# Kernel optimization log

Hardware: AMD Instinct MI355X
Metric: run time of the kernel (lower is better)

The kernel has to match this reference:

```python
import jax, jax.numpy as jnp
import numpy as np

# Elliptical structuring-element sizes (cv2.MORPH_ELLIPSE-like), per init_kwargs.
KERNEL_SIZES = [3, 5, 7]
B, C, H, W = 16, 1, 1024, 1024
_MAX_VAL = 1e4  # kornia's max_val; geodesic border padding uses +-max_val
_EPS = 1e-7     # smp DiceLoss eps


def _ellipse_offsets(k):
    """Offsets (i, j) within a k x k window where the elliptical mask is 1."""
    r = k // 2
    yy, xx = np.mgrid[-r:r + 1, -r:r + 1]
    rr = max(r, 1)
    mask = (xx / rr) ** 2 + (yy / rr) ** 2 <= 1.0 + 1e-9
    return [(i, j) for i in range(k) for j in range(k) if mask[i, j]]


def _morph(x, k, offsets, is_dilation):
    """Flat morphological dilation (max) / erosion (min) over the ellipse support.
    Matches kornia's unfold-based morphology with geodesic border handling,
    but computed as a fused running max/min over static shifted views (no unfold blow-up)."""
    pad = k // 2
    fill = -_MAX_VAL if is_dilation else _MAX_VAL
    xp = jnp.pad(x, ((0, 0), (0, 0), (pad, pad), (pad, pad)), constant_values=fill)
    h, w = x.shape[-2], x.shape[-1]
    op = jnp.maximum if is_dilation else jnp.minimum
    i0, j0 = offsets[0]
    out = xp[..., i0:i0 + h, j0:j0 + w]
    for (i, j) in offsets[1:]:
        out = op(out, xp[..., i:i + h, j:j + w])
    return out


def _dice_loss(pred, target):
    """smp.losses.DiceLoss(mode='binary', from_logits=False): reduce over dims (batch, pixels)."""
    b = pred.shape[0]
    p = pred.reshape(b, 1, -1)
    t = target.reshape(b, 1, -1)
    inter = jnp.sum(p * t, axis=(0, 2))            # [1]
    card = jnp.sum(p + t, axis=(0, 2))             # [1]
    score = 2.0 * inter / jnp.clip(card, _EPS)
    loss = (1.0 - score) * (jnp.sum(t, axis=(0, 2)) > 0)
    return jnp.mean(loss)


def setup_inputs() -> dict:
    key = jax.random.key(0)
    k1, k2 = jax.random.split(key)
    pred = jax.random.uniform(k1, (B, C, H, W), dtype=jnp.float32)
    teacher = jax.random.uniform(k2, (B, C, H, W), dtype=jnp.float32)
    return {"pred_student_prob": pred, "teacher_prob": teacher}


def reference(pred_student_prob, teacher_prob):
    teacher = jax.lax.stop_gradient(teacher_prob)  # .detach()
    total = jnp.float32(0.0)
    for k in KERNEL_SIZES:
        offs = _ellipse_offsets(k)
        obj_dil = _morph(teacher, k, offs, True)
        obj_ero = _morph(teacher, k, offs, False)
        total = total + _dice_loss(pred_student_prob, obj_dil) + _dice_loss(pred_student_prob, obj_ero)
    return total / len(KERNEL_SIZES)
```

## Files before the change

kernel.cpp:

```cpp
#include <hip/hip_runtime.h>

#define H_ 1024
#define W_ 1024
#define B_ 16
#define TH 8
#define STEPS (TH + 6)
#define GX (H_ / TH)
#define NBLK (GX * B_)
#define NACC 13


__global__ __launch_bounds__(256, 2) void k_partials(const float* __restrict__ pred,
                                                     const float* __restrict__ tch,
                                                     float* __restrict__ partials) {
  const int tid = threadIdx.x;
  const int b   = blockIdx.y;
  const int y0  = blockIdx.x * TH;
  const int x0  = tid * 4;
  const float* tb = tch  + (size_t)b * (H_ * W_);
  const float* pb = pred + (size_t)b * (H_ * W_);

  float acc[NACC];
#pragma unroll
  for (int j = 0; j < NACC; j++) acc[j] = 0.f;

  float h0q[7][4];
  float h3M[5][4], h3N[5][4];
  float h5M[6][4], h5N[6][4];
  float h7M[4][4], h7N[4][4];

#pragma unroll
  for (int s = 0; s < STEPS; ++s) {
    const int t    = y0 + s - 3;
    const int trow = t < 0 ? 0 : (t >= H_ ? H_ - 1 : t);
    const float* tr = tb + (size_t)trow * W_;

    float a[12];
    const float4 cv = *reinterpret_cast<const float4*>(tr + x0);
    a[4] = cv.x; a[5] = cv.y; a[6] = cv.z; a[7] = cv.w;
    if (tid > 0) {
      const float4 lv = *reinterpret_cast<const float4*>(tr + x0 - 4);
      a[0] = lv.x; a[1] = lv.y; a[2] = lv.z; a[3] = lv.w;
    } else {
      a[0] = a[1] = a[2] = a[3] = cv.x;
    }
    if (tid < 255) {
      const float4 rv = *reinterpret_cast<const float4*>(tr + x0 + 4);
      a[8] = rv.x; a[9] = rv.y; a[10] = rv.z; a[11] = rv.w;
    } else {
      a[8] = a[9] = a[10] = a[11] = cv.w;
    }

    float QM[8], QN[8];
#pragma unroll
    for (int i = 1; i <= 7; ++i) {
      QM[i] = fmaxf(fmaxf(a[i], a[i + 1]), a[i + 2]);
      QN[i] = fminf(fminf(a[i], a[i + 1]), a[i + 2]);
    }
#pragma unroll
    for (int c = 0; c < 4; ++c) {
      h0q[s % 7][c] = a[c + 4];
      h3M[s % 5][c] = QM[c + 3];
      h3N[s % 5][c] = QN[c + 3];
      h5M[s % 6][c] = fmaxf(QM[c + 2], QM[c + 4]);
      h5N[s % 6][c] = fminf(QN[c + 2], QN[c + 4]);
      h7M[s % 4][c] = fmaxf(fmaxf(QM[c + 1], QM[c + 4]), a[c + 7]);
      h7N[s % 4][c] = fminf(fminf(QN[c + 1], QN[c + 4]), a[c + 7]);
    }

    if (s >= 6) {
      const int j = s - 6;
      const float4 pv = *reinterpret_cast<const float4*>(pb + (size_t)(y0 + j) * W_ + x0);
      const float p[4] = {pv.x, pv.y, pv.z, pv.w};
#pragma unroll
      for (int c = 0; c < 4; ++c) {
        const float d3v = fmaxf(fmaxf(h3M[(s + 2) % 5][c], h0q[(s + 3) % 7][c]), h0q[(s + 5) % 7][c]);
        const float e3v = fminf(fminf(h3N[(s + 2) % 5][c], h0q[(s + 3) % 7][c]), h0q[(s + 5) % 7][c]);

        float d5v = fmaxf(fmaxf(h5M[(s + 3) % 6][c], h3M[(s + 1) % 5][c]), h3M[(s + 3) % 5][c]);
        d5v = fmaxf(fmaxf(d5v, h0q[(s + 2) % 7][c]), h0q[(s + 6) % 7][c]);
        float e5v = fminf(fminf(h5N[(s + 3) % 6][c], h3N[(s + 1) % 5][c]), h3N[(s + 3) % 5][c]);
        e5v = fminf(fminf(e5v, h0q[(s + 2) % 7][c]), h0q[(s + 6) % 7][c]);

        float d7v = fmaxf(fmaxf(h7M[(s + 1) % 4][c], h5M[(s + 2) % 6][c]), h5M[(s + 4) % 6][c]);
        d7v = fmaxf(fmaxf(d7v, h5M[(s + 1) % 6][c]), h5M[(s + 5) % 6][c]);
        d7v = fmaxf(fmaxf(d7v, h0q[(s + 1) % 7][c]), h0q[s % 7][c]);
        float e7v = fminf(fminf(h7N[(s + 1) % 4][c], h5N[(s + 2) % 6][c]), h5N[(s + 4) % 6][c]);
        e7v = fminf(fminf(e7v, h5N[(s + 1) % 6][c]), h5N[(s + 5) % 6][c]);
        e7v = fminf(fminf(e7v, h0q[(s + 1) % 7][c]), h0q[s % 7][c]);

        acc[0]  += p[c];
        acc[1]  += d3v;  acc[2]  = fmaf(p[c], d3v, acc[2]);
        acc[3]  += e3v;  acc[4]  = fmaf(p[c], e3v, acc[4]);
        acc[5]  += d5v;  acc[6]  = fmaf(p[c], d5v, acc[6]);
        acc[7]  += e5v;  acc[8]  = fmaf(p[c], e5v, acc[8]);
        acc[9]  += d7v;  acc[10] = fmaf(p[c], d7v, acc[10]);
        acc[11] += e7v;  acc[12] = fmaf(p[c], e7v, acc[12]);
      }
    }
  }

#pragma unroll
  for (int j = 0; j < NACC; j++) {
    float v = acc[j];
#pragma unroll
    for (int off = 32; off > 0; off >>= 1) v += __shfl_down(v, off, 64);
    acc[j] = v;
  }
  __shared__ float red[4][NACC];
  const int lane = tid & 63, wv = tid >> 6;
  if (lane == 0) {
#pragma unroll
    for (int j = 0; j < NACC; j++) red[wv][j] = acc[j];
  }
  __syncthreads();
  if (tid == 0) {
    const int bid = blockIdx.y * gridDim.x + blockIdx.x;
#pragma unroll
    for (int j = 0; j < NACC; j++)
      partials[bid * NACC + j] = red[0][j] + red[1][j] + red[2][j] + red[3][j];
  }
}

__global__ __launch_bounds__(256) void k_final(const float* __restrict__ partials,
                                               float* __restrict__ out) {
  double acc[NACC];
#pragma unroll
  for (int j = 0; j < NACC; j++) acc[j] = 0.0;
  for (int i = threadIdx.x; i < NBLK; i += 256) {
#pragma unroll
    for (int j = 0; j < NACC; j++) acc[j] += (double)partials[i * NACC + j];
  }
  __shared__ double red[NACC][256];
#pragma unroll
  for (int j = 0; j < NACC; j++) red[j][threadIdx.x] = acc[j];
  __syncthreads();
  for (int s = 128; s > 0; s >>= 1) {
    if (threadIdx.x < (unsigned)s) {
#pragma unroll
      for (int j = 0; j < NACC; j++) red[j][threadIdx.x] += red[j][threadIdx.x + s];
    }
    __syncthreads();
  }
  if (threadIdx.x == 0) {
    const double Sp = red[0][0];
    double total = 0.0;
#pragma unroll
    for (int k = 0; k < 3; k++) {
      const double Sd = red[1 + 4 * k][0], Id = red[2 + 4 * k][0];
      const double Se = red[3 + 4 * k][0], Ie = red[4 + 4 * k][0];
      double cd = Sp + Sd; if (cd < 1e-7) cd = 1e-7;
      double ce = Sp + Se; if (ce < 1e-7) ce = 1e-7;
      total += (1.0 - 2.0 * Id / cd) * (Sd > 0.0 ? 1.0 : 0.0);
      total += (1.0 - 2.0 * Ie / ce) * (Se > 0.0 ? 1.0 : 0.0);
    }
    out[0] = (float)(total / 3.0);
  }
}

extern "C" void kernel_launch(void* const* d_in, const int* in_sizes, int n_in,
                              void* d_out, int out_size, void* d_ws, size_t ws_size,
                              hipStream_t stream) {
  const float* pred = (const float*)d_in[0];
  const float* tch  = (const float*)d_in[1];
  float* partials = (float*)d_ws;

  k_partials<<<dim3(GX, B_), 256, 0, stream>>>(pred, tch, partials);
  k_final<<<1, 256, 0, stream>>>(partials, (float*)d_out);
}
```

Measured before the change: 164.7 us.

## Split dilation and erosion into separate block halves with taller tiles

Dilation and erosion now run in separate blocks, selected by blockIdx.z through a templated body. This halves the live ring-buffer state per thread so launch bounds can allow 4 blocks per SM instead of 2. The tile height doubles to 16 rows, which cuts the halo re-read overhead. In exchange, teacher and pred are each read twice, once per z-slice, which adds memory traffic. Partials are stored column-major, and the final kernel reduces them with direct loads and wave shuffles instead of a shared-memory tree.

```diff
diff --git a/kernel.cpp b/kernel.cpp
--- a/kernel.cpp
+++ b/kernel.cpp
@@ -3,31 +3,30 @@
 #define H_ 1024
 #define W_ 1024
 #define B_ 16
-#define TH 8
+#define TH 16
 #define STEPS (TH + 6)
 #define GX (H_ / TH)
-#define NBLK (GX * B_)
+#define NB2 (GX * B_)
 #define NACC 13
 
+template<bool M>
+__device__ __forceinline__ float O2(float a, float b) { return M ? fmaxf(a, b) : fminf(a, b); }
+template<bool M>
+__device__ __forceinline__ float O3(float a, float b, float c) {
+  return M ? fmaxf(fmaxf(a, b), c) : fminf(fminf(a, b), c);
+}
 
-__global__ __launch_bounds__(256, 2) void k_partials(const float* __restrict__ pred,
-                                                     const float* __restrict__ tch,
-                                                     float* __restrict__ partials) {
-  const int tid = threadIdx.x;
-  const int b   = blockIdx.y;
-  const int y0  = blockIdx.x * TH;
-  const int x0  = tid * 4;
-  const float* tb = tch  + (size_t)b * (H_ * W_);
-  const float* pb = pred + (size_t)b * (H_ * W_);
+template<bool M>
+__device__ __forceinline__ void morph_body(const float* __restrict__ pb,
+                                           const float* __restrict__ tb,
+                                           float* __restrict__ partials,
+                                           int tid, int y0, int bid) {
+  const int x0 = tid * 4;
+  float acc[7];
+#pragma unroll
+  for (int j = 0; j < 7; j++) acc[j] = 0.f;
 
-  float acc[NACC];
-#pragma unroll
-  for (int j = 0; j < NACC; j++) acc[j] = 0.f;
-
-  float h0q[7][4];
-  float h3M[5][4], h3N[5][4];
-  float h5M[6][4], h5N[6][4];
-  float h7M[4][4], h7N[4][4];
+  float h0q[7][4], h3q[5][4], h5q[6][4], h7q[4][4];
 
 #pragma unroll
   for (int s = 0; s < STEPS; ++s) {
@@ -51,63 +50,101 @@
       a[8] = a[9] = a[10] = a[11] = cv.w;
     }
 
-    float QM[8], QN[8];
+    float Q[8];
 #pragma unroll
-    for (int i = 1; i <= 7; ++i) {
-      QM[i] = fmaxf(fmaxf(a[i], a[i + 1]), a[i + 2]);
-      QN[i] = fminf(fminf(a[i], a[i + 1]), a[i + 2]);
-    }
+    for (int i = 1; i <= 7; ++i) Q[i] = O3<M>(a[i], a[i + 1], a[i + 2]);
 #pragma unroll
     for (int c = 0; c < 4; ++c) {
       h0q[s % 7][c] = a[c + 4];
-      h3M[s % 5][c] = QM[c + 3];
-      h3N[s % 5][c] = QN[c + 3];
-      h5M[s % 6][c] = fmaxf(QM[c + 2], QM[c + 4]);
-      h5N[s % 6][c] = fminf(QN[c + 2], QN[c + 4]);
-      h7M[s % 4][c] = fmaxf(fmaxf(QM[c + 1], QM[c + 4]), a[c + 7]);
-      h7N[s % 4][c] = fminf(fminf(QN[c + 1], QN[c + 4]), a[c + 7]);
+      h3q[s % 5][c] = Q[c + 3];
+      h5q[s % 6][c] = O2<M>(Q[c + 2], Q[c + 4]);
+      h7q[s % 4][c] = O3<M>(Q[c + 1], Q[c + 4], a[c + 7]);
     }
 
     if (s >= 6) {
-      const int j = s - 6;
-      const float4 pv = *reinterpret_cast<const float4*>(pb + (size_t)(y0 + j) * W_ + x0);
+      const float4 pv = *reinterpret_cast<const float4*>(pb + (size_t)(y0 + s - 6) * W_ + x0);
       const float p[4] = {pv.x, pv.y, pv.z, pv.w};
 #pragma unroll
       for (int c = 0; c < 4; ++c) {
-        const float d3v = fmaxf(fmaxf(h3M[(s + 2) % 5][c], h0q[(s + 3) % 7][c]), h0q[(s + 5) % 7][c]);
-        const float e3v = fminf(fminf(h3N[(s + 2) % 5][c], h0q[(s + 3) % 7][c]), h0q[(s + 5) % 7][c]);
+        const float k3 = O3<M>(h3q[(s + 2) % 5][c], h0q[(s + 3) % 7][c], h0q[(s + 5) % 7][c]);
+        float k5 = O3<M>(h5q[(s + 3) % 6][c], h3q[(s + 1) % 5][c], h3q[(s + 3) % 5][c]);
+        k5 = O3<M>(k5, h0q[(s + 2) % 7][c], h0q[(s + 6) % 7][c]);
+        float k7 = O3<M>(h7q[(s + 1) % 4][c], h5q[(s + 2) % 6][c], h5q[(s + 4) % 6][c]);
+        k7 = O3<M>(k7, h5q[(s + 1) % 6][c], h5q[(s + 5) % 6][c]);
+        k7 = O3<M>(k7, h0q[(s + 1) % 7][c], h0q[s % 7][c]);
 
-        float d5v = fmaxf(fmaxf(h5M[(s + 3) % 6][c], h3M[(s + 1) % 5][c]), h3M[(s + 3) % 5][c]);
-        d5v = fmaxf(fmaxf(d5v, h0q[(s + 2) % 7][c]), h0q[(s + 6) % 7][c]);
-        float e5v = fminf(fminf(h5N[(s + 3) % 6][c], h3N[(s + 1) % 5][c]), h3N[(s + 3) % 5][c]);
-        e5v = fminf(fminf(e5v, h0q[(s + 2) % 7][c]), h0q[(s + 6) % 7][c]);
-
-        float d7v = fmaxf(fmaxf(h7M[(s + 1) % 4][c], h5M[(s + 2) % 6][c]), h5M[(s + 4) % 6][c]);
-        d7v = fmaxf(fmaxf(d7v, h5M[(s + 1) % 6][c]), h5M[(s + 5) % 6][c]);
-        d7v = fmaxf(fmaxf(d7v, h0q[(s + 1) % 7][c]), h0q[s % 7][c]);
-        float e7v = fminf(fminf(h7N[(s + 1) % 4][c], h5N[(s + 2) % 6][c]), h5N[(s + 4) % 6][c]);
-        e7v = fminf(fminf(e7v, h5N[(s + 1) % 6][c]), h5N[(s + 5) % 6][c]);
-        e7v = fminf(fminf(e7v, h0q[(s + 1) % 7][c]), h0q[s % 7][c]);
-
-        acc[0]  += p[c];
-        acc[1]  += d3v;  acc[2]  = fmaf(p[c], d3v, acc[2]);
-        acc[3]  += e3v;  acc[4]  = fmaf(p[c], e3v, acc[4]);
-        acc[5]  += d5v;  acc[6]  = fmaf(p[c], d5v, acc[6]);
-        acc[7]  += e5v;  acc[8]  = fmaf(p[c], e5v, acc[8]);
-        acc[9]  += d7v;  acc[10] = fmaf(p[c], d7v, acc[10]);
-        acc[11] += e7v;  acc[12] = fmaf(p[c], e7v, acc[12]);
+        if (M) acc[0] += p[c];
+        acc[1] += k3;  acc[2] = fmaf(p[c], k3, acc[2]);
+        acc[3] += k5;  acc[4] = fmaf(p[c], k5, acc[4]);
+        acc[5] += k7;  acc[6] = fmaf(p[c], k7, acc[6]);
       }
     }
   }
 
 #pragma unroll
-  for (int j = 0; j < NACC; j++) {
+  for (int j = 0; j < 7; j++) {
     float v = acc[j];
 #pragma unroll
     for (int off = 32; off > 0; off >>= 1) v += __shfl_down(v, off, 64);
     acc[j] = v;
   }
-  __shared__ float red[4][NACC];
+  __shared__ float red[4][7];
+  const int lane = tid & 63, wv = tid >> 6;
+  if (lane == 0) {
+#pragma unroll
+    for (int j = 0; j < 7; j++) red[wv][j] = acc[j];
+  }
+  __syncthreads();
+  if (tid == 0) {
+    float tot[7];
+#pragma unroll
+    for (int j = 0; j < 7; j++) tot[j] = red[0][j] + red[1][j] + red[2][j] + red[3][j];
+    if (M) {
+      partials[0 * NB2 + bid]  = tot[0];
+      partials[1 * NB2 + bid]  = tot[1];  partials[2 * NB2 + bid]  = tot[2];
+      partials[5 * NB2 + bid]  = tot[3];  partials[6 * NB2 + bid]  = tot[4];
+      partials[9 * NB2 + bid]  = tot[5];  partials[10 * NB2 + bid] = tot[6];
+    } else {
+      partials[3 * NB2 + bid]  = tot[1];  partials[4 * NB2 + bid]  = tot[2];
+      partials[7 * NB2 + bid]  = tot[3];  partials[8 * NB2 + bid]  = tot[4];
+      partials[11 * NB2 + bid] = tot[5];  partials[12 * NB2 + bid] = tot[6];
+    }
+  }
+}
+
+__global__ __launch_bounds__(256, 4) void k_partials(const float* __restrict__ pred,
+                                                     const float* __restrict__ tch,
+                                                     float* __restrict__ partials) {
+  const int b   = blockIdx.y;
+  const int y0  = blockIdx.x * TH;
+  const int bid = blockIdx.y * GX + blockIdx.x;
+  const float* tb = tch  + (size_t)b * (H_ * W_);
+  const float* pb = pred + (size_t)b * (H_ * W_);
+  if (blockIdx.z == 0) morph_body<true >(pb, tb, partials, threadIdx.x, y0, bid);
+  else                 morph_body<false>(pb, tb, partials, threadIdx.x, y0, bid);
+}
+
+__global__ __launch_bounds__(256) void k_final(const float* __restrict__ partials,
+                                               float* __restrict__ out) {
+  const int tid = threadIdx.x;
+  float v[NACC][4];
+#pragma unroll
+  for (int j = 0; j < NACC; j++)
+#pragma unroll
+    for (int k = 0; k < 4; k++)
+      v[j][k] = partials[j * NB2 + tid + k * 256];
+
+  double acc[NACC];
+#pragma unroll
+  for (int j = 0; j < NACC; j++)
+    acc[j] = ((double)v[j][0] + v[j][1]) + ((double)v[j][2] + v[j][3]);
+
+#pragma unroll
+  for (int j = 0; j < NACC; j++) {
+#pragma unroll
+    for (int off = 32; off > 0; off >>= 1) acc[j] += __shfl_down(acc[j], off, 64);
+  }
+  __shared__ double red[4][NACC];
   const int lane = tid & 63, wv = tid >> 6;
   if (lane == 0) {
 #pragma unroll
@@ -115,40 +152,15 @@
   }
   __syncthreads();
   if (tid == 0) {
-    const int bid = blockIdx.y * gridDim.x + blockIdx.x;
+    double t_[NACC];
 #pragma unroll
-    for (int j = 0; j < NACC; j++)
-      partials[bid * NACC + j] = red[0][j] + red[1][j] + red[2][j] + red[3][j];
-  }
-}
-
-__global__ __launch_bounds__(256) void k_final(const float* __restrict__ partials,
-                                               float* __restrict__ out) {
-  double acc[NACC];
-#pragma unroll
-  for (int j = 0; j < NACC; j++) acc[j] = 0.0;
-  for (int i = threadIdx.x; i < NBLK; i += 256) {
-#pragma unroll
-    for (int j = 0; j < NACC; j++) acc[j] += (double)partials[i * NACC + j];
-  }
-  __shared__ double red[NACC][256];
-#pragma unroll
-  for (int j = 0; j < NACC; j++) red[j][threadIdx.x] = acc[j];
-  __syncthreads();
-  for (int s = 128; s > 0; s >>= 1) {
-    if (threadIdx.x < (unsigned)s) {
-#pragma unroll
-      for (int j = 0; j < NACC; j++) red[j][threadIdx.x] += red[j][threadIdx.x + s];
-    }
-    __syncthreads();
-  }
-  if (threadIdx.x == 0) {
-    const double Sp = red[0][0];
+    for (int j = 0; j < NACC; j++) t_[j] = red[0][j] + red[1][j] + red[2][j] + red[3][j];
+    const double Sp = t_[0];
     double total = 0.0;
 #pragma unroll
     for (int k = 0; k < 3; k++) {
-      const double Sd = red[1 + 4 * k][0], Id = red[2 + 4 * k][0];
-      const double Se = red[3 + 4 * k][0], Ie = red[4 + 4 * k][0];
+      const double Sd = t_[1 + 4 * k], Id = t_[2 + 4 * k];
+      const double Se = t_[3 + 4 * k], Ie = t_[4 + 4 * k];
       double cd = Sp + Sd; if (cd < 1e-7) cd = 1e-7;
       double ce = Sp + Se; if (ce < 1e-7) ce = 1e-7;
       total += (1.0 - 2.0 * Id / cd) * (Sd > 0.0 ? 1.0 : 0.0);
@@ -165,6 +177,6 @@
   const float* tch  = (const float*)d_in[1];
   float* partials = (float*)d_ws;
 
-  k_partials<<<dim3(GX, B_), 256, 0, stream>>>(pred, tch, partials);
+  k_partials<<<dim3(GX, B_, 2), 256, 0, stream>>>(pred, tch, partials);
   k_final<<<1, 256, 0, stream>>>(partials, (float*)d_out);
 }
```

After: 397.6 us. +141.4%, slower.

## Stage teacher and pred rows through double-buffered LDS via direct global-to-LDS loads

Applied to the files above, without the earlier changes.

The main kernel now loads each teacher row and pred row straight into shared memory with the global_load_lds builtin. Loads are double-buffered so the next row is fetched while the current one is processed, and neighbours read their halo from LDS instead of issuing three global float4 loads. This adds a block barrier every step. The partials layout becomes column-major so the final kernel reads it coalesced, and the final reduction switches from a shared-memory tree to wave shuffles.

```diff
diff --git a/kernel.cpp b/kernel.cpp
--- a/kernel.cpp
+++ b/kernel.cpp
@@ -1,4 +1,5 @@
 #include <hip/hip_runtime.h>
+#include <stdint.h>
 
 #define H_ 1024
 #define W_ 1024
@@ -9,14 +10,25 @@
 #define NBLK (GX * B_)
 #define NACC 13
 
+__device__ __forceinline__ void gl2lds16(const float* g, float* l) {
+  __builtin_amdgcn_global_load_lds(
+      (const __attribute__((address_space(1))) void*)g,
+      (__attribute__((address_space(3))) void*)l,
+      16, 0, 0);
+}
 
 __global__ __launch_bounds__(256, 2) void k_partials(const float* __restrict__ pred,
                                                      const float* __restrict__ tch,
                                                      float* __restrict__ partials) {
+  __shared__ float tbuf[2][1032];
+  __shared__ float qbuf[2][1024];
+  __shared__ float red[4][NACC];
+
   const int tid = threadIdx.x;
   const int b   = blockIdx.y;
   const int y0  = blockIdx.x * TH;
   const int x0  = tid * 4;
+  const int wv  = tid >> 6;
   const float* tb = tch  + (size_t)b * (H_ * W_);
   const float* pb = pred + (size_t)b * (H_ * W_);
 
@@ -29,27 +41,28 @@
   float h5M[6][4], h5N[6][4];
   float h7M[4][4], h7N[4][4];
 
+  {
+    const int t = y0 - 3;
+    const int trow = t < 0 ? 0 : t;
+    gl2lds16(tb + (size_t)trow * W_ + x0, &tbuf[0][4 + (wv << 8)]);
+  }
+  __syncthreads();
+
 #pragma unroll
   for (int s = 0; s < STEPS; ++s) {
-    const int t    = y0 + s - 3;
-    const int trow = t < 0 ? 0 : (t >= H_ ? H_ - 1 : t);
-    const float* tr = tb + (size_t)trow * W_;
+    if (s + 1 < STEPS) {
+      const int t = y0 + s + 1 - 3;
+      const int trow = t < 0 ? 0 : (t >= H_ ? H_ - 1 : t);
+      gl2lds16(tb + (size_t)trow * W_ + x0, &tbuf[(s + 1) & 1][4 + (wv << 8)]);
+      if (s >= 5)
+        gl2lds16(pb + (size_t)(y0 + s - 5) * W_ + x0, &qbuf[(s + 1) & 1][wv << 8]);
+    }
 
-    float a[12];
-    const float4 cv = *reinterpret_cast<const float4*>(tr + x0);
-    a[4] = cv.x; a[5] = cv.y; a[6] = cv.z; a[7] = cv.w;
-    if (tid > 0) {
-      const float4 lv = *reinterpret_cast<const float4*>(tr + x0 - 4);
-      a[0] = lv.x; a[1] = lv.y; a[2] = lv.z; a[3] = lv.w;
-    } else {
-      a[0] = a[1] = a[2] = a[3] = cv.x;
-    }
-    if (tid < 255) {
-      const float4 rv = *reinterpret_cast<const float4*>(tr + x0 + 4);
-      a[8] = rv.x; a[9] = rv.y; a[10] = rv.z; a[11] = rv.w;
-    } else {
-      a[8] = a[9] = a[10] = a[11] = cv.w;
-    }
+    const float4* t4 = reinterpret_cast<const float4*>(&tbuf[s & 1][x0]);
+    const float4 A0 = t4[0], A1 = t4[1], A2 = t4[2];
+    float a[12] = {A0.x, A0.y, A0.z, A0.w, A1.x, A1.y, A1.z, A1.w, A2.x, A2.y, A2.z, A2.w};
+    if (tid == 0)   { a[0] = a[1] = a[2]  = a[3]  = a[4]; }
+    if (tid == 255) { a[8] = a[9] = a[10] = a[11] = a[7]; }
 
     float QM[8], QN[8];
 #pragma unroll
@@ -69,8 +82,7 @@
     }
 
     if (s >= 6) {
-      const int j = s - 6;
-      const float4 pv = *reinterpret_cast<const float4*>(pb + (size_t)(y0 + j) * W_ + x0);
+      const float4 pv = *reinterpret_cast<const float4*>(&qbuf[s & 1][x0]);
       const float p[4] = {pv.x, pv.y, pv.z, pv.w};
 #pragma unroll
       for (int c = 0; c < 4; ++c) {
@@ -98,6 +110,8 @@
         acc[11] += e7v;  acc[12] = fmaf(p[c], e7v, acc[12]);
       }
     }
+
+    __syncthreads();
   }
 
 #pragma unroll
@@ -107,8 +121,7 @@
     for (int off = 32; off > 0; off >>= 1) v += __shfl_down(v, off, 64);
     acc[j] = v;
   }
-  __shared__ float red[4][NACC];
-  const int lane = tid & 63, wv = tid >> 6;
+  const int lane = tid & 63;
   if (lane == 0) {
 #pragma unroll
     for (int j = 0; j < NACC; j++) red[wv][j] = acc[j];
@@ -118,37 +131,44 @@
     const int bid = blockIdx.y * gridDim.x + blockIdx.x;
 #pragma unroll
     for (int j = 0; j < NACC; j++)
-      partials[bid * NACC + j] = red[0][j] + red[1][j] + red[2][j] + red[3][j];
+      partials[j * NBLK + bid] = red[0][j] + red[1][j] + red[2][j] + red[3][j];
   }
 }
 
 __global__ __launch_bounds__(256) void k_final(const float* __restrict__ partials,
                                                float* __restrict__ out) {
+  const int tid = threadIdx.x;
   double acc[NACC];
 #pragma unroll
   for (int j = 0; j < NACC; j++) acc[j] = 0.0;
-  for (int i = threadIdx.x; i < NBLK; i += 256) {
 #pragma unroll
-    for (int j = 0; j < NACC; j++) acc[j] += (double)partials[i * NACC + j];
+  for (int k = 0; k < NBLK / 256; k++) {
+#pragma unroll
+    for (int j = 0; j < NACC; j++)
+      acc[j] += (double)partials[j * NBLK + tid + k * 256];
   }
-  __shared__ double red[NACC][256];
 #pragma unroll
-  for (int j = 0; j < NACC; j++) red[j][threadIdx.x] = acc[j];
+  for (int j = 0; j < NACC; j++) {
+#pragma unroll
+    for (int off = 32; off > 0; off >>= 1) acc[j] += __shfl_down(acc[j], off, 64);
+  }
+  __shared__ double red[4][NACC];
+  const int lane = tid & 63, wv = tid >> 6;
+  if (lane == 0) {
+#pragma unroll
+    for (int j = 0; j < NACC; j++) red[wv][j] = acc[j];
+  }
   __syncthreads();
-  for (int s = 128; s > 0; s >>= 1) {
-    if (threadIdx.x < (unsigned)s) {
+  if (tid == 0) {
+    double t_[NACC];
 #pragma unroll
-      for (int j = 0; j < NACC; j++) red[j][threadIdx.x] += red[j][threadIdx.x + s];
-    }
-    __syncthreads();
-  }
-  if (threadIdx.x == 0) {
-    const double Sp = red[0][0];
+    for (int j = 0; j < NACC; j++) t_[j] = red[0][j] + red[1][j] + red[2][j] + red[3][j];
+    const double Sp = t_[0];
     double total = 0.0;
 #pragma unroll
     for (int k = 0; k < 3; k++) {
-      const double Sd = red[1 + 4 * k][0], Id = red[2 + 4 * k][0];
-      const double Se = red[3 + 4 * k][0], Ie = red[4 + 4 * k][0];
+      const double Sd = t_[1 + 4 * k], Id = t_[2 + 4 * k];
+      const double Se = t_[3 + 4 * k], Ie = t_[4 + 4 * k];
       double cd = Sp + Sd; if (cd < 1e-7) cd = 1e-7;
       double ce = Sp + Se; if (ce < 1e-7) ce = 1e-7;
       total += (1.0 - 2.0 * Id / cd) * (Sd > 0.0 ? 1.0 : 0.0);
```

Measured after the change: 232.6 us. 1.41x slower.

## Replace two-stage partial reduction with global atomics and remap tiles across XCDs

Applied to the files above, without the earlier changes.

Each block now atomically adds its 13 accumulators into a small zeroed global buffer, padded to stride 16. Before, it wrote per-block partials that a 256-thread final kernel reduced in double. The final kernel shrinks to one wavefront reading the 13 sums. Block indices are also remapped so that consecutive blocks go to different row tiles, likely to spread L2 locality across XCDs. The changes add a memset launch and float atomic accumulation, which loses the double-precision summation and makes the result order-dependent.

```diff
diff --git a/kernel.cpp b/kernel.cpp
--- a/kernel.cpp
+++ b/kernel.cpp
@@ -6,17 +6,19 @@
 #define TH 8
 #define STEPS (TH + 6)
 #define GX (H_ / TH)
-#define NBLK (GX * B_)
 #define NACC 13
+#define ACC_STRIDE 16
 
 
 __global__ __launch_bounds__(256, 2) void k_partials(const float* __restrict__ pred,
                                                      const float* __restrict__ tch,
-                                                     float* __restrict__ partials) {
+                                                     float* __restrict__ accum) {
   const int tid = threadIdx.x;
-  const int b   = blockIdx.y;
-  const int y0  = blockIdx.x * TH;
-  const int x0  = tid * 4;
+  const int n     = blockIdx.y * gridDim.x + blockIdx.x;
+  const int b     = n >> 7;
+  const int ytile = (n & 7) * 16 + ((n >> 3) & 15);
+  const int y0    = ytile * TH;
+  const int x0    = tid * 4;
   const float* tb = tch  + (size_t)b * (H_ * W_);
   const float* pb = pred + (size_t)b * (H_ * W_);
 
@@ -114,41 +116,24 @@
     for (int j = 0; j < NACC; j++) red[wv][j] = acc[j];
   }
   __syncthreads();
-  if (tid == 0) {
-    const int bid = blockIdx.y * gridDim.x + blockIdx.x;
-#pragma unroll
-    for (int j = 0; j < NACC; j++)
-      partials[bid * NACC + j] = red[0][j] + red[1][j] + red[2][j] + red[3][j];
-  }
+  if (tid < NACC)
+    atomicAdd(&accum[tid * ACC_STRIDE],
+              red[0][tid] + red[1][tid] + red[2][tid] + red[3][tid]);
 }
 
-__global__ __launch_bounds__(256) void k_final(const float* __restrict__ partials,
-                                               float* __restrict__ out) {
-  double acc[NACC];
+__global__ void k_final(const float* __restrict__ accum, float* __restrict__ out) {
+  const int lane = threadIdx.x;
+  const float v = (lane < NACC) ? accum[lane * ACC_STRIDE] : 0.f;
+  double t_[NACC];
 #pragma unroll
-  for (int j = 0; j < NACC; j++) acc[j] = 0.0;
-  for (int i = threadIdx.x; i < NBLK; i += 256) {
-#pragma unroll
-    for (int j = 0; j < NACC; j++) acc[j] += (double)partials[i * NACC + j];
-  }
-  __shared__ double red[NACC][256];
-#pragma unroll
-  for (int j = 0; j < NACC; j++) red[j][threadIdx.x] = acc[j];
-  __syncthreads();
-  for (int s = 128; s > 0; s >>= 1) {
-    if (threadIdx.x < (unsigned)s) {
-#pragma unroll
-      for (int j = 0; j < NACC; j++) red[j][threadIdx.x] += red[j][threadIdx.x + s];
-    }
-    __syncthreads();
-  }
-  if (threadIdx.x == 0) {
-    const double Sp = red[0][0];
+  for (int j = 0; j < NACC; j++) t_[j] = (double)__shfl(v, j, 64);
+  if (lane == 0) {
+    const double Sp = t_[0];
     double total = 0.0;
 #pragma unroll
     for (int k = 0; k < 3; k++) {
-      const double Sd = red[1 + 4 * k][0], Id = red[2 + 4 * k][0];
-      const double Se = red[3 + 4 * k][0], Ie = red[4 + 4 * k][0];
+      const double Sd = t_[1 + 4 * k], Id = t_[2 + 4 * k];
+      const double Se = t_[3 + 4 * k], Ie = t_[4 + 4 * k];
       double cd = Sp + Sd; if (cd < 1e-7) cd = 1e-7;
       double ce = Sp + Se; if (ce < 1e-7) ce = 1e-7;
       total += (1.0 - 2.0 * Id / cd) * (Sd > 0.0 ? 1.0 : 0.0);
@@ -163,8 +148,9 @@
                               hipStream_t stream) {
   const float* pred = (const float*)d_in[0];
   const float* tch  = (const float*)d_in[1];
-  float* partials = (float*)d_ws;
+  float* accum = (float*)d_ws;
 
-  k_partials<<<dim3(GX, B_), 256, 0, stream>>>(pred, tch, partials);
-  k_final<<<1, 256, 0, stream>>>(partials, (float*)d_out);
+  hipMemsetAsync(accum, 0, NACC * ACC_STRIDE * sizeof(float), stream);
+  k_partials<<<dim3(GX, B_), 256, 0, stream>>>(pred, tch, accum);
+  k_final<<<1, 64, 0, stream>>>(accum, (float*)d_out);
 }
```

Result: slower. 179.4 us (+8.9%).
